# Kernel tuning notes

Hardware: AMD Instinct MI355X
Metric: run time of the kernel (lower is better)

Reference implementation:

```python
import jax, jax.numpy as jnp
import numpy as np

MAX_ITER = 10
EPS = 1e-4


def setup_inputs() -> dict:
    key = jax.random.key(0)
    k1, k2, k3 = jax.random.split(key, 3)
    B, N, M = 64, 1024, 1024
    s = jax.random.uniform(k1, (B, N, M), dtype=jnp.float32)
    # valid row/col counts per batch element, kept >= N//2 (and >=1) to avoid degenerate empty slices
    nrows = jax.random.randint(k2, (B,), N // 2, N + 1, dtype=jnp.int32)
    ncols = jax.random.randint(k3, (B,), M // 2, M + 1, dtype=jnp.int32)
    return {"s": s, "nrows": nrows, "ncols": ncols}


def reference(s, nrows, ncols):
    """Masked Sinkhorn: alternating column/row normalization restricted to the
    per-batch valid [0:nrows[b], 0:ncols[b]] block; out-of-range entries are zeroed.
    Matches torch loop: even iter normalizes by column sums over valid rows,
    odd iter by row sums over valid cols (each sum taken over the epsilon-augmented s).
    """
    B, N, M = s.shape
    row_mask = (jnp.arange(N)[None, :] < nrows[:, None]).astype(s.dtype)  # [B, N]
    col_mask = (jnp.arange(M)[None, :] < ncols[:, None]).astype(s.dtype)  # [B, M]
    valid = row_mask[:, :, None] * col_mask[:, None, :]                   # [B, N, M]

    s = s + EPS
    for i in range(MAX_ITER):
        if i % 2 == 1:
            # row sums over valid columns -> [B, N, 1]
            denom = jnp.einsum('bm,bnm->bn', col_mask, s)[:, :, None]
        else:
            # column sums over valid rows -> [B, 1, M]
            denom = jnp.einsum('bn,bnm->bm', row_mask, s)[:, None, :]
        denom = jnp.where(denom == 0, 1.0, denom)  # guard empty slices
        s = jnp.where(valid > 0, s / denom, 0.0)
    return s
```

## Files before the change

kernel.cpp:

```cpp
#include <hip/hip_runtime.h>
#include <hip/hip_fp16.h>


namespace {
constexpr int B_ = 64;
constexpr int N_ = 1024;
constexpr int M_ = 1024;
constexpr float EPS_ = 1e-4f;
constexpr int PCHUNK = 16;
constexpr int RPC = N_ / PCHUNK;
}

typedef float f32x4_ __attribute__((ext_vector_type(4)));

__device__ __forceinline__ float4 nt_load4(const float* p) {
    f32x4_ v = __builtin_nontemporal_load(reinterpret_cast<const f32x4_*>(p));
    return float4{v.x, v.y, v.z, v.w};
}

__global__ void prep_pass(const float* __restrict__ s,
                          __half* __restrict__ q,
                          float* __restrict__ partial,
                          const int* __restrict__ nrows,
                          const int* __restrict__ ncols) {
    __shared__ float lds[4][M_];
    const int b = blockIdx.y, p = blockIdx.x;
    const int nr = nrows[b], nc = ncols[b];
    const int wave = threadIdx.x >> 6, lane = threadIdx.x & 63;

    float4 ca[4];
#pragma unroll
    for (int t = 0; t < 4; ++t) ca[t] = float4{0.f, 0.f, 0.f, 0.f};

    const int rbeg = p * RPC + wave * 16;
    const int rend = min(rbeg + 16, nr);
    const float* sb = s + (size_t)b * N_ * M_;
    __half* qb = q + (size_t)b * N_ * M_;

    for (int n = rbeg; n < rend; ++n) {
#pragma unroll
        for (int t = 0; t < 4; ++t) {
            const int m0 = t * 256 + lane * 4;
            float4 v = {0.f, 0.f, 0.f, 0.f};
            if (m0 < nc) {
                v = nt_load4(sb + (size_t)n * M_ + m0);
                v.x += EPS_; v.y += EPS_; v.z += EPS_; v.w += EPS_;
            }
            __half2 h01 = __floats2half2_rn(v.x, v.y);
            __half2 h23 = __floats2half2_rn(v.z, v.w);
            uint2 st;
            st.x = *reinterpret_cast<const unsigned*>(&h01);
            st.y = *reinterpret_cast<const unsigned*>(&h23);
            *reinterpret_cast<uint2*>(qb + (size_t)n * M_ + m0) = st;
            ca[t].x += v.x; ca[t].y += v.y; ca[t].z += v.z; ca[t].w += v.w;
        }
    }
#pragma unroll
    for (int t = 0; t < 4; ++t)
        *reinterpret_cast<float4*>(&lds[wave][t * 256 + lane * 4]) = ca[t];
    __syncthreads();
    const int m0 = threadIdx.x * 4;
    float4 a0 = *reinterpret_cast<const float4*>(&lds[0][m0]);
    float4 a1 = *reinterpret_cast<const float4*>(&lds[1][m0]);
    float4 a2 = *reinterpret_cast<const float4*>(&lds[2][m0]);
    float4 a3 = *reinterpret_cast<const float4*>(&lds[3][m0]);
    float4 o;
    o.x = a0.x + a1.x + a2.x + a3.x;
    o.y = a0.y + a1.y + a2.y + a3.y;
    o.z = a0.z + a1.z + a2.z + a3.z;
    o.w = a0.w + a1.w + a2.w + a3.w;
    *reinterpret_cast<float4*>(partial + ((size_t)b * PCHUNK + p) * M_ + m0) = o;
}

__global__ void fused_pass_h(const __half* __restrict__ q,
                             const float* __restrict__ partial_in,
                             float* __restrict__ partial_out,
                             const int* __restrict__ nrows,
                             const int* __restrict__ ncols) {
    __shared__ float lds[4][M_];
    const int b = blockIdx.y, p = blockIdx.x;
    const int nr = nrows[b], nc = ncols[b];
    const int wave = threadIdx.x >> 6, lane = threadIdx.x & 63;

    {
        const int m0 = threadIdx.x * 4;
        const float* pp = partial_in + (size_t)b * PCHUNK * M_ + m0;
        float4 sacc = {0.f, 0.f, 0.f, 0.f};
#pragma unroll
        for (int i = 0; i < PCHUNK; ++i) {
            const float4 v = *reinterpret_cast<const float4*>(pp + (size_t)i * M_);
            sacc.x += v.x; sacc.y += v.y; sacc.z += v.z; sacc.w += v.w;
        }
        float4 cv;
        cv.x = (sacc.x == 0.f) ? 1.f : 1.f / sacc.x;
        cv.y = (sacc.y == 0.f) ? 1.f : 1.f / sacc.y;
        cv.z = (sacc.z == 0.f) ? 1.f : 1.f / sacc.z;
        cv.w = (sacc.w == 0.f) ? 1.f : 1.f / sacc.w;
        *reinterpret_cast<float4*>(&lds[0][m0]) = cv;
    }
    __syncthreads();

    float cm[16];
#pragma unroll
    for (int t = 0; t < 2; ++t)
#pragma unroll
        for (int j = 0; j < 8; ++j) {
            const int m = t * 512 + lane * 8 + j;
            const float v = lds[0][m];
            cm[t * 8 + j] = (m < nc) ? v : 0.f;
        }
    __syncthreads();

    float ca[16];
#pragma unroll
    for (int k = 0; k < 16; ++k) ca[k] = 0.f;

    const int rbeg = p * RPC + wave * 16;
    const int rend = min(rbeg + 16, nr);
    const __half* qb = q + (size_t)b * N_ * M_;

    for (int n = rbeg; n < rend; ++n) {
        float f[16];
#pragma unroll
        for (int t = 0; t < 2; ++t) {
            const float4 raw = *reinterpret_cast<const float4*>(
                qb + (size_t)n * M_ + t * 512 + lane * 8);
            const __half2* hp = reinterpret_cast<const __half2*>(&raw);
#pragma unroll
            for (int k = 0; k < 4; ++k) {
                const float2 fr = __half22float2(hp[k]);
                f[t * 8 + 2 * k] = fr.x;
                f[t * 8 + 2 * k + 1] = fr.y;
            }
        }
        float acc = 0.f;
#pragma unroll
        for (int k = 0; k < 16; ++k) acc = fmaf(f[k], cm[k], acc);
#pragma unroll
        for (int off = 1; off < 64; off <<= 1)
            acc += __shfl_xor(acc, off, 64);
        const float rn = 1.f / acc;
#pragma unroll
        for (int k = 0; k < 16; ++k) ca[k] = fmaf(f[k], rn, ca[k]);
    }

#pragma unroll
    for (int t = 0; t < 2; ++t) {
        float4 v0 = {ca[t * 8 + 0], ca[t * 8 + 1], ca[t * 8 + 2], ca[t * 8 + 3]};
        float4 v1 = {ca[t * 8 + 4], ca[t * 8 + 5], ca[t * 8 + 6], ca[t * 8 + 7]};
        *reinterpret_cast<float4*>(&lds[wave][t * 512 + lane * 8]) = v0;
        *reinterpret_cast<float4*>(&lds[wave][t * 512 + lane * 8 + 4]) = v1;
    }
    __syncthreads();
    const int m0 = threadIdx.x * 4;
    float4 a0 = *reinterpret_cast<const float4*>(&lds[0][m0]);
    float4 a1 = *reinterpret_cast<const float4*>(&lds[1][m0]);
    float4 a2 = *reinterpret_cast<const float4*>(&lds[2][m0]);
    float4 a3 = *reinterpret_cast<const float4*>(&lds[3][m0]);
    float4 o;
    o.x = a0.x + a1.x + a2.x + a3.x;
    o.y = a0.y + a1.y + a2.y + a3.y;
    o.z = a0.z + a1.z + a2.z + a3.z;
    o.w = a0.w + a1.w + a2.w + a3.w;
    *reinterpret_cast<float4*>(partial_out + ((size_t)b * PCHUNK + p) * M_ + m0) = o;
}

__global__ void final_pass_h(const __half* __restrict__ q,
                             const float* __restrict__ partial_in,
                             float* __restrict__ out,
                             const int* __restrict__ nrows,
                             const int* __restrict__ ncols) {
    __shared__ float ldsc[M_];
    const int b = blockIdx.y, p = blockIdx.x;
    const int nr = nrows[b], nc = ncols[b];
    const int wave = threadIdx.x >> 6, lane = threadIdx.x & 63;

    {
        const int m0 = threadIdx.x * 4;
        const float* pp = partial_in + (size_t)b * PCHUNK * M_ + m0;
        float4 sacc = {0.f, 0.f, 0.f, 0.f};
#pragma unroll
        for (int i = 0; i < PCHUNK; ++i) {
            const float4 v = *reinterpret_cast<const float4*>(pp + (size_t)i * M_);
            sacc.x += v.x; sacc.y += v.y; sacc.z += v.z; sacc.w += v.w;
        }
        float4 cv;
        cv.x = (sacc.x == 0.f) ? 1.f : 1.f / sacc.x;
        cv.y = (sacc.y == 0.f) ? 1.f : 1.f / sacc.y;
        cv.z = (sacc.z == 0.f) ? 1.f : 1.f / sacc.z;
        cv.w = (sacc.w == 0.f) ? 1.f : 1.f / sacc.w;
        *reinterpret_cast<float4*>(&ldsc[m0]) = cv;
    }
    __syncthreads();

    float cm[16];
#pragma unroll
    for (int t = 0; t < 2; ++t)
#pragma unroll
        for (int j = 0; j < 8; ++j) {
            const int m = t * 512 + lane * 8 + j;
            const float v = ldsc[m];
            cm[t * 8 + j] = (m < nc) ? v : 0.f;
        }

    const int rbeg = p * RPC + wave * 16;
    const __half* qb = q + (size_t)b * N_ * M_;
    float* ob = out + (size_t)b * N_ * M_;

    for (int n = rbeg; n < rbeg + 16; ++n) {
        if (n >= nr) {
            const float4 z = {0.f, 0.f, 0.f, 0.f};
#pragma unroll
            for (int t = 0; t < 2; ++t) {
                *reinterpret_cast<float4*>(ob + (size_t)n * M_ + t * 512 + lane * 8) = z;
                *reinterpret_cast<float4*>(ob + (size_t)n * M_ + t * 512 + lane * 8 + 4) = z;
            }
            continue;
        }
        float f[16];
#pragma unroll
        for (int t = 0; t < 2; ++t) {
            const float4 raw = *reinterpret_cast<const float4*>(
                qb + (size_t)n * M_ + t * 512 + lane * 8);
            const __half2* hp = reinterpret_cast<const __half2*>(&raw);
#pragma unroll
            for (int k = 0; k < 4; ++k) {
                const float2 fr = __half22float2(hp[k]);
                f[t * 8 + 2 * k] = fr.x;
                f[t * 8 + 2 * k + 1] = fr.y;
            }
        }
        float acc = 0.f;
#pragma unroll
        for (int k = 0; k < 16; ++k) acc = fmaf(f[k], cm[k], acc);
#pragma unroll
        for (int off = 1; off < 64; off <<= 1)
            acc += __shfl_xor(acc, off, 64);
        const float rn = 1.f / acc;
#pragma unroll
        for (int t = 0; t < 2; ++t) {
            float4 o0, o1;
            o0.x = f[t * 8 + 0] * rn * cm[t * 8 + 0];
            o0.y = f[t * 8 + 1] * rn * cm[t * 8 + 1];
            o0.z = f[t * 8 + 2] * rn * cm[t * 8 + 2];
            o0.w = f[t * 8 + 3] * rn * cm[t * 8 + 3];
            o1.x = f[t * 8 + 4] * rn * cm[t * 8 + 4];
            o1.y = f[t * 8 + 5] * rn * cm[t * 8 + 5];
            o1.z = f[t * 8 + 6] * rn * cm[t * 8 + 6];
            o1.w = f[t * 8 + 7] * rn * cm[t * 8 + 7];
            *reinterpret_cast<float4*>(ob + (size_t)n * M_ + t * 512 + lane * 8) = o0;
            *reinterpret_cast<float4*>(ob + (size_t)n * M_ + t * 512 + lane * 8 + 4) = o1;
        }
    }
}

extern "C" void kernel_launch(void* const* d_in, const int* in_sizes, int n_in,
                              void* d_out, int out_size, void* d_ws, size_t ws_size,
                              hipStream_t stream) {
    const float* s = (const float*)d_in[0];
    const int* nrows = (const int*)d_in[1];
    const int* ncols = (const int*)d_in[2];
    float* out = (float*)d_out;

    const size_t qbytes = (size_t)B_ * N_ * M_ * sizeof(__half);
    __half* q = (__half*)d_ws;
    float* pa = (float*)((char*)d_ws + qbytes);
    float* pb = pa + (size_t)B_ * PCHUNK * M_;

    const dim3 blk(256);
    const dim3 g_chunk(PCHUNK, B_);

    prep_pass<<<g_chunk, blk, 0, stream>>>(s, q, pa, nrows, ncols);
    fused_pass_h<<<g_chunk, blk, 0, stream>>>(q, pa, pb, nrows, ncols);
    fused_pass_h<<<g_chunk, blk, 0, stream>>>(q, pb, pa, nrows, ncols);
    fused_pass_h<<<g_chunk, blk, 0, stream>>>(q, pa, pb, nrows, ncols);
    fused_pass_h<<<g_chunk, blk, 0, stream>>>(q, pb, pa, nrows, ncols);
    final_pass_h<<<g_chunk, blk, 0, stream>>>(q, pa, out, nrows, ncols);
}
```

Before: 230.5 us.

## Merge six pass launches into one cooperative persistent kernel with grid syncs

Moves the prep, fused and final pass bodies into device functions and runs them inside a single cooperative kernel. Blocks loop over virtual (batch, chunk) tiles, and grid.sync() separates the phases. This removes five kernel launch boundaries and their tail effects. In exchange it pays grid-wide barrier costs and per-call host occupancy and attribute queries, and the grid size is capped by occupancy, so a block may process several tiles in sequence. The old multi-launch path is kept as a fallback.

```diff
diff --git a/kernel.cpp b/kernel.cpp
--- a/kernel.cpp
+++ b/kernel.cpp
@@ -1,5 +1,8 @@
 #include <hip/hip_runtime.h>
 #include <hip/hip_fp16.h>
+#include <hip/hip_cooperative_groups.h>
+
+namespace cg = cooperative_groups;
 
 
 namespace {
@@ -9,6 +12,7 @@
 constexpr float EPS_ = 1e-4f;
 constexpr int PCHUNK = 16;
 constexpr int RPC = N_ / PCHUNK;
+constexpr int NVB = PCHUNK * B_;
 }
 
 typedef float f32x4_ __attribute__((ext_vector_type(4)));
@@ -18,13 +22,14 @@
     return float4{v.x, v.y, v.z, v.w};
 }
 
-__global__ void prep_pass(const float* __restrict__ s,
-                          __half* __restrict__ q,
-                          float* __restrict__ partial,
-                          const int* __restrict__ nrows,
-                          const int* __restrict__ ncols) {
-    __shared__ float lds[4][M_];
-    const int b = blockIdx.y, p = blockIdx.x;
+
+__device__ __forceinline__ void prep_body(int b, int p,
+                                          const float* __restrict__ s,
+                                          __half* __restrict__ q,
+                                          float* __restrict__ partial,
+                                          const int* __restrict__ nrows,
+                                          const int* __restrict__ ncols,
+                                          float (*lds)[M_]) {
     const int nr = nrows[b], nc = ncols[b];
     const int wave = threadIdx.x >> 6, lane = threadIdx.x & 63;
 
@@ -55,15 +60,16 @@
             ca[t].x += v.x; ca[t].y += v.y; ca[t].z += v.z; ca[t].w += v.w;
         }
     }
+    __syncthreads();
 #pragma unroll
     for (int t = 0; t < 4; ++t)
         *reinterpret_cast<float4*>(&lds[wave][t * 256 + lane * 4]) = ca[t];
     __syncthreads();
     const int m0 = threadIdx.x * 4;
-    float4 a0 = *reinterpret_cast<const float4*>(&lds[0][m0]);
-    float4 a1 = *reinterpret_cast<const float4*>(&lds[1][m0]);
-    float4 a2 = *reinterpret_cast<const float4*>(&lds[2][m0]);
-    float4 a3 = *reinterpret_cast<const float4*>(&lds[3][m0]);
+    const float4 a0 = *reinterpret_cast<const float4*>(&lds[0][m0]);
+    const float4 a1 = *reinterpret_cast<const float4*>(&lds[1][m0]);
+    const float4 a2 = *reinterpret_cast<const float4*>(&lds[2][m0]);
+    const float4 a3 = *reinterpret_cast<const float4*>(&lds[3][m0]);
     float4 o;
     o.x = a0.x + a1.x + a2.x + a3.x;
     o.y = a0.y + a1.y + a2.y + a3.y;
@@ -72,16 +78,17 @@
     *reinterpret_cast<float4*>(partial + ((size_t)b * PCHUNK + p) * M_ + m0) = o;
 }
 
-__global__ void fused_pass_h(const __half* __restrict__ q,
-                             const float* __restrict__ partial_in,
-                             float* __restrict__ partial_out,
-                             const int* __restrict__ nrows,
-                             const int* __restrict__ ncols) {
-    __shared__ float lds[4][M_];
-    const int b = blockIdx.y, p = blockIdx.x;
+__device__ __forceinline__ void fused_body(int b, int p,
+                                           const __half* __restrict__ q,
+                                           const float* __restrict__ partial_in,
+                                           float* __restrict__ partial_out,
+                                           const int* __restrict__ nrows,
+                                           const int* __restrict__ ncols,
+                                           float (*lds)[M_]) {
     const int nr = nrows[b], nc = ncols[b];
     const int wave = threadIdx.x >> 6, lane = threadIdx.x & 63;
 
+    __syncthreads();
     {
         const int m0 = threadIdx.x * 4;
         const float* pp = partial_in + (size_t)b * PCHUNK * M_ + m0;
@@ -153,10 +160,10 @@
     }
     __syncthreads();
     const int m0 = threadIdx.x * 4;
-    float4 a0 = *reinterpret_cast<const float4*>(&lds[0][m0]);
-    float4 a1 = *reinterpret_cast<const float4*>(&lds[1][m0]);
-    float4 a2 = *reinterpret_cast<const float4*>(&lds[2][m0]);
-    float4 a3 = *reinterpret_cast<const float4*>(&lds[3][m0]);
+    const float4 a0 = *reinterpret_cast<const float4*>(&lds[0][m0]);
+    const float4 a1 = *reinterpret_cast<const float4*>(&lds[1][m0]);
+    const float4 a2 = *reinterpret_cast<const float4*>(&lds[2][m0]);
+    const float4 a3 = *reinterpret_cast<const float4*>(&lds[3][m0]);
     float4 o;
     o.x = a0.x + a1.x + a2.x + a3.x;
     o.y = a0.y + a1.y + a2.y + a3.y;
@@ -165,16 +172,17 @@
     *reinterpret_cast<float4*>(partial_out + ((size_t)b * PCHUNK + p) * M_ + m0) = o;
 }
 
-__global__ void final_pass_h(const __half* __restrict__ q,
-                             const float* __restrict__ partial_in,
-                             float* __restrict__ out,
-                             const int* __restrict__ nrows,
-                             const int* __restrict__ ncols) {
-    __shared__ float ldsc[M_];
-    const int b = blockIdx.y, p = blockIdx.x;
+__device__ __forceinline__ void final_body(int b, int p,
+                                           const __half* __restrict__ q,
+                                           const float* __restrict__ partial_in,
+                                           float* __restrict__ out,
+                                           const int* __restrict__ nrows,
+                                           const int* __restrict__ ncols,
+                                           float* ldsc) {
     const int nr = nrows[b], nc = ncols[b];
     const int wave = threadIdx.x >> 6, lane = threadIdx.x & 63;
 
+    __syncthreads();
     {
         const int m0 = threadIdx.x * 4;
         const float* pp = partial_in + (size_t)b * PCHUNK * M_ + m0;
@@ -254,6 +262,54 @@
     }
 }
 
+__global__ void __launch_bounds__(256, 4)
+sink_coop(const float* __restrict__ s, __half* __restrict__ q,
+          float* __restrict__ pa, float* __restrict__ pb,
+          float* __restrict__ out, const int* __restrict__ nrows,
+          const int* __restrict__ ncols) {
+    __shared__ float lds[4][M_];
+    cg::grid_group grid = cg::this_grid();
+
+    for (int vb = blockIdx.x; vb < NVB; vb += gridDim.x)
+        prep_body(vb >> 4, vb & 15, s, q, pa, nrows, ncols, lds);
+    grid.sync();
+    for (int vb = blockIdx.x; vb < NVB; vb += gridDim.x)
+        fused_body(vb >> 4, vb & 15, q, pa, pb, nrows, ncols, lds);
+    grid.sync();
+    for (int vb = blockIdx.x; vb < NVB; vb += gridDim.x)
+        fused_body(vb >> 4, vb & 15, q, pb, pa, nrows, ncols, lds);
+    grid.sync();
+    for (int vb = blockIdx.x; vb < NVB; vb += gridDim.x)
+        fused_body(vb >> 4, vb & 15, q, pa, pb, nrows, ncols, lds);
+    grid.sync();
+    for (int vb = blockIdx.x; vb < NVB; vb += gridDim.x)
+        fused_body(vb >> 4, vb & 15, q, pb, pa, nrows, ncols, lds);
+    grid.sync();
+    for (int vb = blockIdx.x; vb < NVB; vb += gridDim.x)
+        final_body(vb >> 4, vb & 15, q, pa, out, nrows, ncols, lds[0]);
+}
+
+__global__ void prep_pass(const float* __restrict__ s, __half* __restrict__ q,
+                          float* __restrict__ partial,
+                          const int* __restrict__ nrows, const int* __restrict__ ncols) {
+    __shared__ float lds[4][M_];
+    prep_body(blockIdx.y, blockIdx.x, s, q, partial, nrows, ncols, lds);
+}
+__global__ void fused_pass_h(const __half* __restrict__ q,
+                             const float* __restrict__ partial_in,
+                             float* __restrict__ partial_out,
+                             const int* __restrict__ nrows, const int* __restrict__ ncols) {
+    __shared__ float lds[4][M_];
+    fused_body(blockIdx.y, blockIdx.x, q, partial_in, partial_out, nrows, ncols, lds);
+}
+__global__ void final_pass_h(const __half* __restrict__ q,
+                             const float* __restrict__ partial_in,
+                             float* __restrict__ out,
+                             const int* __restrict__ nrows, const int* __restrict__ ncols) {
+    __shared__ float ldsc[M_];
+    final_body(blockIdx.y, blockIdx.x, q, partial_in, out, nrows, ncols, ldsc);
+}
+
 extern "C" void kernel_launch(void* const* d_in, const int* in_sizes, int n_in,
                               void* d_out, int out_size, void* d_ws, size_t ws_size,
                               hipStream_t stream) {
@@ -267,13 +323,31 @@
     float* pa = (float*)((char*)d_ws + qbytes);
     float* pb = pa + (size_t)B_ * PCHUNK * M_;
 
-    const dim3 blk(256);
-    const dim3 g_chunk(PCHUNK, B_);
-
-    prep_pass<<<g_chunk, blk, 0, stream>>>(s, q, pa, nrows, ncols);
-    fused_pass_h<<<g_chunk, blk, 0, stream>>>(q, pa, pb, nrows, ncols);
-    fused_pass_h<<<g_chunk, blk, 0, stream>>>(q, pb, pa, nrows, ncols);
-    fused_pass_h<<<g_chunk, blk, 0, stream>>>(q, pa, pb, nrows, ncols);
-    fused_pass_h<<<g_chunk, blk, 0, stream>>>(q, pb, pa, nrows, ncols);
-    final_pass_h<<<g_chunk, blk, 0, stream>>>(q, pa, out, nrows, ncols);
-}
+    int dev = 0;
+    hipError_t e0 = hipGetDevice(&dev);
+    int ncu = 0;
+    hipError_t e1 = hipDeviceGetAttribute(&ncu, hipDeviceAttributeMultiprocessorCount, dev);
+    int maxbpc = 0;
+    hipError_t e2 = hipOccupancyMaxActiveBlocksPerMultiprocessor(&maxbpc, sink_coop, 256, 0);
+    const bool qok = (e0 == hipSuccess) && (e1 == hipSuccess) && (e2 == hipSuccess);
+    const long cap = qok ? (long)maxbpc * (long)ncu : 0;
+
+    if (cap >= 256) {
+        const int G = (int)((cap < (long)NVB) ? cap : (long)NVB);
+        void* args[] = {(void*)&s, (void*)&q, (void*)&pa, (void*)&pb,
+                        (void*)&out, (void*)&nrows, (void*)&ncols};
+        hipError_t e3 = hipLaunchCooperativeKernel((void*)sink_coop, dim3(G), dim3(256),
+                                                   args, 0, stream);
+        if (e3 == hipSuccess) return;
+    }
+    {
+        const dim3 blk(256);
+        const dim3 g_chunk(PCHUNK, B_);
+        prep_pass<<<g_chunk, blk, 0, stream>>>(s, q, pa, nrows, ncols);
+        fused_pass_h<<<g_chunk, blk, 0, stream>>>(q, pa, pb, nrows, ncols);
+        fused_pass_h<<<g_chunk, blk, 0, stream>>>(q, pb, pa, nrows, ncols);
+        fused_pass_h<<<g_chunk, blk, 0, stream>>>(q, pa, pb, nrows, ncols);
+        fused_pass_h<<<g_chunk, blk, 0, stream>>>(q, pb, pa, nrows, ncols);
+        final_pass_h<<<g_chunk, blk, 0, stream>>>(q, pa, out, nrows, ncols);
+    }
+}
```

Result: slower. 559.3 us (+142.6%).
